# Performance work log

Measured on AMD Instinct MI355X. Metric: run time of the kernel, lower is better.

Reference implementation:

```python
import jax, jax.numpy as jnp
import numpy as np

OUT_FEATURES = 8192
IN_FEATURES = 8192
BATCH = 512


def setup_inputs() -> dict:
    key = jax.random.key(0)
    k_x, k_w, k_s = jax.random.split(key, 3)
    x = jax.random.normal(k_x, (BATCH, IN_FEATURES), dtype=jnp.float32)
    # packed int4 weights: each int holds two nibbles (values 0..255)
    packed_weight = jax.random.randint(k_w, (OUT_FEATURES, IN_FEATURES // 2), 0, 256, dtype=jnp.int32)
    # per-output-row scale (positive, as produced by abs-max quantization)
    scale = jax.random.uniform(k_s, (OUT_FEATURES, 1), dtype=jnp.float32) * 0.02 + 1e-4
    return {"x": x, "packed_weight": packed_weight, "scale": scale}


def reference(x, packed_weight, scale):
    # Unpack two 4-bit values per byte: high nibble first (matches torch loop:
    # col i <- packed >> 4 & 15, col i+1 <- packed & 15), then subtract zero-point 8.
    hi = (packed_weight >> 4) & 15
    lo = packed_weight & 15
    q = jnp.stack([hi, lo], axis=-1).reshape(OUT_FEATURES, IN_FEATURES) - 8  # [out, in] int
    w = q.astype(scale.dtype) * scale  # dequantized weight [out, in]
    # linear: y = x @ W^T
    return jnp.einsum('bi,oi->bo', x, w)
```

## Files before the change

### kernel.cpp

```cpp
#include <hip/hip_runtime.h>
#include <cstdint>
#include <cstddef>

#define IN_F 8192
#define OUT_F 8192
#define BATCH 512
#define KSPLIT 4
#define KSLICE (IN_F / KSPLIT)
#define BK 64
#define TILES (KSLICE / BK)
#define BM 256
#define BN 256

typedef __bf16 bf16x8 __attribute__((ext_vector_type(8)));
typedef float floatx4 __attribute__((ext_vector_type(4)));

__device__ __forceinline__ ushort f2bf(float f) {
  uint32_t u = __float_as_uint(f);
  u += 0x7FFFu + ((u >> 16) & 1u);
  return (ushort)(u >> 16);
}

__device__ __forceinline__ uint32_t dq(int p) {
  uint32_t u = (uint32_t)p;
  return (((u >> 4) & 0xFu) | ((u & 0xFu) << 16)) | 0x43004300u;
}

__device__ __forceinline__ void gl16(const void* g, uint32_t* l) {
  __builtin_amdgcn_global_load_lds(
      (const __attribute__((address_space(1))) uint32_t*)g,
      (__attribute__((address_space(3))) uint32_t*)l, 16, 0, 0);
}

__global__ __launch_bounds__(256) void cvt_rowsum(const float* __restrict__ x,
                                                  ushort* __restrict__ xb,
                                                  float* __restrict__ rowsum,
                                                  float* __restrict__ out) {
  const int b = blockIdx.x;
  const int t = threadIdx.x;
  const float4* xr = (const float4*)(x + (size_t)b * IN_F);
  ushort4* xo = (ushort4*)(xb + (size_t)b * IN_F);
  float4 z = {0.f, 0.f, 0.f, 0.f};
  float4* orow = (float4*)(out + (size_t)b * OUT_F);
  float s[4] = {0.f, 0.f, 0.f, 0.f};
#pragma unroll
  for (int i = 0; i < 8; ++i) {
    float4 v = xr[i * 256 + t];
    ushort4 o;
    o.x = f2bf(v.x); o.y = f2bf(v.y); o.z = f2bf(v.z); o.w = f2bf(v.w);
    xo[i * 256 + t] = o;
    orow[i * 256 + t] = z;
    s[i >> 1] += __uint_as_float((uint32_t)o.x << 16) + __uint_as_float((uint32_t)o.y << 16)
               + __uint_as_float((uint32_t)o.z << 16) + __uint_as_float((uint32_t)o.w << 16);
  }
  __shared__ float red[4][4];
  const int lane = t & 63, wid = t >> 6;
#pragma unroll
  for (int j = 0; j < 4; ++j) {
    float v = s[j];
#pragma unroll
    for (int off = 32; off >= 1; off >>= 1) v += __shfl_down(v, off, 64);
    if (lane == 0) red[wid][j] = v;
  }
  __syncthreads();
  if (t < 4) rowsum[t * BATCH + b] = red[0][t] + red[1][t] + red[2][t] + red[3][t];
}

__global__ __launch_bounds__(512, 2) void qgemm(const ushort* __restrict__ xb,
                                                const int* __restrict__ pw,
                                                const float* __restrict__ scale,
                                                const float* __restrict__ rowsum,
                                                float* __restrict__ out) {
  __shared__ uint32_t As[2 * BM * 32];
  __shared__ uint32_t Bs[2 * BN * 32];

  const int tid = threadIdx.x;
  const int lane = tid & 63;
  const int w = tid >> 6;
  const int wm = w >> 2, wn = w & 3;
  const int lr = lane & 15, lq = lane >> 4;

  const int n0 = blockIdx.x * BN;
  const int m0 = blockIdx.y * BM;
  const int ks = blockIdx.z;

  const char* aSrc = (const char*)xb
      + (size_t)(m0 + w * 32 + (lane >> 3)) * (IN_F * 2)
      + (size_t)ks * (KSLICE * 2)
      + (size_t)((((lane & 7) ^ ((lane >> 3) & 7)) * 16));
  uint32_t* aDst = As + (w * 32) * 32;

  const int rt = tid >> 1;
  const int c0 = (tid & 1) * 2;
  const int rk = rt & 7;
  const int* bSrc = pw + (size_t)(n0 + rt) * (IN_F / 2) + ks * (KSLICE / 2);

  const int key = lr & 7;
  const int aOff = (wm * 128 + lr) * 32 + ((lq ^ key) * 4);
  const int bOff = (wn * 64 + lr) * 32 + ((lq ^ key) * 4);

  floatx4 acc[8][4] = {};

  auto stB = [&](int nb, int q, int4 p) {
    int4 u;
    u.x = dq(p.x); u.y = dq(p.y); u.z = dq(p.z); u.w = dq(p.w);
    *(int4*)(Bs + nb * 8192 + rt * 32 + ((q ^ rk) * 4)) = u;
  };

#define RD_BV(kh)                                                            \
  _Pragma("unroll") for (int fn = 0; fn < 4; ++fn)                           \
      bv[fn] = *(const bf16x8*)(Bs + (((bOff + fn * 512) ^ ((kh)*16)) + buf * 8192));
#define RD_AV(mh, kh)                                                        \
  _Pragma("unroll") for (int fm = 0; fm < 4; ++fm)                           \
      av[fm] = *(const bf16x8*)(As + (((aOff + (mh)*2048 + fm * 512) ^ ((kh)*16)) + buf * 8192));
#define MFMA_BLK(mh)                                                         \
  __builtin_amdgcn_s_setprio(1);                                             \
  _Pragma("unroll") for (int fm = 0; fm < 4; ++fm)                           \
      _Pragma("unroll") for (int fn = 0; fn < 4; ++fn)                       \
          acc[(mh)*4 + fm][fn] = __builtin_amdgcn_mfma_f32_16x16x32_bf16(    \
              av[fm], bv[fn], acc[(mh)*4 + fm][fn], 0, 0, 0);                \
  __builtin_amdgcn_s_setprio(0);

  {
    int4 p0 = *(const int4*)(bSrc + c0 * 4);
    int4 p1 = *(const int4*)(bSrc + c0 * 4 + 4);
    int4 p2 = *(const int4*)(bSrc + (c0 + 4) * 4);
    int4 p3 = *(const int4*)(bSrc + (c0 + 4) * 4 + 4);
    stB(0, c0, p0); stB(0, c0 + 1, p1); stB(0, c0 + 4, p2); stB(0, c0 + 5, p3);
    gl16(aSrc, aDst);
    gl16(aSrc + 131072, aDst + 256);
    gl16(aSrc + 262144, aDst + 512);
    gl16(aSrc + 393216, aDst + 768);
    asm volatile("s_waitcnt lgkmcnt(0)" ::: "memory");
  }

  for (int t = 0; t < TILES - 1; ++t) {
    const int buf = t & 1, nb = buf ^ 1;
    const int* bs = bSrc + (t + 1) * 32;
    int4 pb0 = *(const int4*)(bs + c0 * 4);
    int4 pb1 = *(const int4*)(bs + c0 * 4 + 4);
    int4 pb2 = *(const int4*)(bs + (c0 + 4) * 4);
    int4 pb3 = *(const int4*)(bs + (c0 + 4) * 4 + 4);
    const char* as = aSrc + (size_t)(t + 1) * 128;
    gl16(as, aDst + nb * 8192);
    gl16(as + 131072, aDst + nb * 8192 + 256);
    gl16(as + 262144, aDst + nb * 8192 + 512);
    gl16(as + 393216, aDst + nb * 8192 + 768);
    asm volatile("s_waitcnt vmcnt(8)" ::: "memory");
    asm volatile("s_barrier" ::: "memory");

    bf16x8 av[4], bv[4];
    RD_BV(0);
    RD_AV(0, 0); MFMA_BLK(0);
    stB(nb, c0, pb0); stB(nb, c0 + 1, pb1);
    RD_AV(1, 0); MFMA_BLK(1);
    RD_BV(1);
    RD_AV(0, 1); MFMA_BLK(0);
    stB(nb, c0 + 4, pb2); stB(nb, c0 + 5, pb3);
    RD_AV(1, 1); MFMA_BLK(1);

    asm volatile("s_waitcnt lgkmcnt(0)" ::: "memory");
    asm volatile("s_barrier" ::: "memory");
  }

  {
    const int buf = (TILES - 1) & 1;
    asm volatile("s_waitcnt vmcnt(0)" ::: "memory");
    asm volatile("s_barrier" ::: "memory");
    bf16x8 av[4], bv[4];
    RD_BV(0);
    RD_AV(0, 0); MFMA_BLK(0);
    RD_AV(1, 0); MFMA_BLK(1);
    RD_BV(1);
    RD_AV(0, 1); MFMA_BLK(0);
    RD_AV(1, 1); MFMA_BLK(1);
  }

  const int omb = m0 + wm * 128 + lq * 4;
  const int on = n0 + wn * 64 + lr;
  float scv[4];
#pragma unroll
  for (int fn = 0; fn < 4; ++fn) scv[fn] = scale[on + fn * 16];
  float rsv[8][4];
#pragma unroll
  for (int fmg = 0; fmg < 8; ++fmg)
#pragma unroll
    for (int rr = 0; rr < 4; ++rr)
      rsv[fmg][rr] = rowsum[ks * BATCH + omb + fmg * 16 + rr];

#pragma unroll
  for (int fmg = 0; fmg < 8; ++fmg)
#pragma unroll
    for (int fn = 0; fn < 4; ++fn) {
      const float s = scv[fn];
      float* op = out + (size_t)(omb + fmg * 16) * OUT_F + (on + fn * 16);
#pragma unroll
      for (int rr = 0; rr < 4; ++rr)
        atomicAdd(op + (size_t)rr * OUT_F, s * (acc[fmg][fn][rr] - 136.f * rsv[fmg][rr]));
    }
#undef RD_BV
#undef RD_AV
#undef MFMA_BLK
}

extern "C" void kernel_launch(void* const* d_in, const int* in_sizes, int n_in,
                              void* d_out, int out_size, void* d_ws, size_t ws_size,
                              hipStream_t stream) {
  const float* x = (const float*)d_in[0];
  const int* pw = (const int*)d_in[1];
  const float* scale = (const float*)d_in[2];
  float* out = (float*)d_out;

  ushort* xb = (ushort*)d_ws;
  float* rowsum = (float*)((char*)d_ws + (size_t)BATCH * IN_F * sizeof(ushort));

  cvt_rowsum<<<BATCH, 256, 0, stream>>>(x, xb, rowsum, out);
  dim3 grid(OUT_F / BN, BATCH / BM, KSPLIT);
  qgemm<<<grid, 512, 0, stream>>>(xb, pw, scale, rowsum, out);
}
```

Measured before the change: 302.4 us.

## Replace split-K atomics with plain partial stores and separate reduction kernel

```diff
diff --git a/kernel.cpp b/kernel.cpp
--- a/kernel.cpp
+++ b/kernel.cpp
@@ -5,11 +5,11 @@
 #define IN_F 8192
 #define OUT_F 8192
 #define BATCH 512
-#define KSPLIT 4
+#define KSPLIT 2
 #define KSLICE (IN_F / KSPLIT)
 #define BK 64
 #define TILES (KSLICE / BK)
-#define BM 256
+#define BM 128
 #define BN 256
 
 typedef __bf16 bf16x8 __attribute__((ext_vector_type(8)));
@@ -35,42 +35,44 @@
 __global__ __launch_bounds__(256) void cvt_rowsum(const float* __restrict__ x,
                                                   ushort* __restrict__ xb,
                                                   float* __restrict__ rowsum,
-                                                  float* __restrict__ out) {
+                                                  float* __restrict__ zout) {
   const int b = blockIdx.x;
   const int t = threadIdx.x;
   const float4* xr = (const float4*)(x + (size_t)b * IN_F);
   ushort4* xo = (ushort4*)(xb + (size_t)b * IN_F);
-  float4 z = {0.f, 0.f, 0.f, 0.f};
-  float4* orow = (float4*)(out + (size_t)b * OUT_F);
-  float s[4] = {0.f, 0.f, 0.f, 0.f};
+  float s[2] = {0.f, 0.f};
 #pragma unroll
   for (int i = 0; i < 8; ++i) {
     float4 v = xr[i * 256 + t];
     ushort4 o;
     o.x = f2bf(v.x); o.y = f2bf(v.y); o.z = f2bf(v.z); o.w = f2bf(v.w);
     xo[i * 256 + t] = o;
-    orow[i * 256 + t] = z;
-    s[i >> 1] += __uint_as_float((uint32_t)o.x << 16) + __uint_as_float((uint32_t)o.y << 16)
+    if (zout) {
+      float4 z = {0.f, 0.f, 0.f, 0.f};
+      ((float4*)(zout + (size_t)b * OUT_F))[i * 256 + t] = z;
+    }
+    s[i >> 2] += __uint_as_float((uint32_t)o.x << 16) + __uint_as_float((uint32_t)o.y << 16)
                + __uint_as_float((uint32_t)o.z << 16) + __uint_as_float((uint32_t)o.w << 16);
   }
-  __shared__ float red[4][4];
+  __shared__ float red[4][2];
   const int lane = t & 63, wid = t >> 6;
 #pragma unroll
-  for (int j = 0; j < 4; ++j) {
+  for (int j = 0; j < 2; ++j) {
     float v = s[j];
 #pragma unroll
     for (int off = 32; off >= 1; off >>= 1) v += __shfl_down(v, off, 64);
     if (lane == 0) red[wid][j] = v;
   }
   __syncthreads();
-  if (t < 4) rowsum[t * BATCH + b] = red[0][t] + red[1][t] + red[2][t] + red[3][t];
+  if (t < 2) rowsum[t * BATCH + b] = red[0][t] + red[1][t] + red[2][t] + red[3][t];
 }
 
 __global__ __launch_bounds__(512, 2) void qgemm(const ushort* __restrict__ xb,
                                                 const int* __restrict__ pw,
                                                 const float* __restrict__ scale,
                                                 const float* __restrict__ rowsum,
-                                                float* __restrict__ out) {
+                                                float* __restrict__ out,
+                                                float* __restrict__ part) {
   __shared__ uint32_t As[2 * BM * 32];
   __shared__ uint32_t Bs[2 * BN * 32];
 
@@ -85,10 +87,10 @@
   const int ks = blockIdx.z;
 
   const char* aSrc = (const char*)xb
-      + (size_t)(m0 + w * 32 + (lane >> 3)) * (IN_F * 2)
+      + (size_t)(m0 + w * 16 + (lane >> 3)) * (IN_F * 2)
       + (size_t)ks * (KSLICE * 2)
       + (size_t)((((lane & 7) ^ ((lane >> 3) & 7)) * 16));
-  uint32_t* aDst = As + (w * 32) * 32;
+  uint32_t* aDst = As + (w * 16) * 32;
 
   const int rt = tid >> 1;
   const int c0 = (tid & 1) * 2;
@@ -96,10 +98,10 @@
   const int* bSrc = pw + (size_t)(n0 + rt) * (IN_F / 2) + ks * (KSLICE / 2);
 
   const int key = lr & 7;
-  const int aOff = (wm * 128 + lr) * 32 + ((lq ^ key) * 4);
+  const int aOff = (wm * 64 + lr) * 32 + ((lq ^ key) * 4);
   const int bOff = (wn * 64 + lr) * 32 + ((lq ^ key) * 4);
 
-  floatx4 acc[8][4] = {};
+  floatx4 acc[4][4] = {};
 
   auto stB = [&](int nb, int q, int4 p) {
     int4 u;
@@ -110,15 +112,15 @@
 #define RD_BV(kh)                                                            \
   _Pragma("unroll") for (int fn = 0; fn < 4; ++fn)                           \
       bv[fn] = *(const bf16x8*)(Bs + (((bOff + fn * 512) ^ ((kh)*16)) + buf * 8192));
-#define RD_AV(mh, kh)                                                        \
+#define RD_AV(kh)                                                            \
   _Pragma("unroll") for (int fm = 0; fm < 4; ++fm)                           \
-      av[fm] = *(const bf16x8*)(As + (((aOff + (mh)*2048 + fm * 512) ^ ((kh)*16)) + buf * 8192));
-#define MFMA_BLK(mh)                                                         \
+      av[fm] = *(const bf16x8*)(As + (((aOff + fm * 512) ^ ((kh)*16)) + buf * 4096));
+#define MFMA_BLK()                                                           \
   __builtin_amdgcn_s_setprio(1);                                             \
   _Pragma("unroll") for (int fm = 0; fm < 4; ++fm)                           \
       _Pragma("unroll") for (int fn = 0; fn < 4; ++fn)                       \
-          acc[(mh)*4 + fm][fn] = __builtin_amdgcn_mfma_f32_16x16x32_bf16(    \
-              av[fm], bv[fn], acc[(mh)*4 + fm][fn], 0, 0, 0);                \
+          acc[fm][fn] = __builtin_amdgcn_mfma_f32_16x16x32_bf16(             \
+              av[fm], bv[fn], acc[fm][fn], 0, 0, 0);                         \
   __builtin_amdgcn_s_setprio(0);
 
   {
@@ -129,8 +131,6 @@
     stB(0, c0, p0); stB(0, c0 + 1, p1); stB(0, c0 + 4, p2); stB(0, c0 + 5, p3);
     gl16(aSrc, aDst);
     gl16(aSrc + 131072, aDst + 256);
-    gl16(aSrc + 262144, aDst + 512);
-    gl16(aSrc + 393216, aDst + 768);
     asm volatile("s_waitcnt lgkmcnt(0)" ::: "memory");
   }
 
@@ -142,22 +142,18 @@
     int4 pb2 = *(const int4*)(bs + (c0 + 4) * 4);
     int4 pb3 = *(const int4*)(bs + (c0 + 4) * 4 + 4);
     const char* as = aSrc + (size_t)(t + 1) * 128;
-    gl16(as, aDst + nb * 8192);
-    gl16(as + 131072, aDst + nb * 8192 + 256);
-    gl16(as + 262144, aDst + nb * 8192 + 512);
-    gl16(as + 393216, aDst + nb * 8192 + 768);
-    asm volatile("s_waitcnt vmcnt(8)" ::: "memory");
+    gl16(as, aDst + nb * 4096);
+    gl16(as + 131072, aDst + nb * 4096 + 256);
+    asm volatile("s_waitcnt vmcnt(6)" ::: "memory");
     asm volatile("s_barrier" ::: "memory");
 
     bf16x8 av[4], bv[4];
-    RD_BV(0);
-    RD_AV(0, 0); MFMA_BLK(0);
+    RD_BV(0); RD_AV(0);
+    MFMA_BLK();
+    RD_BV(1); RD_AV(1);
+    MFMA_BLK();
     stB(nb, c0, pb0); stB(nb, c0 + 1, pb1);
-    RD_AV(1, 0); MFMA_BLK(1);
-    RD_BV(1);
-    RD_AV(0, 1); MFMA_BLK(0);
     stB(nb, c0 + 4, pb2); stB(nb, c0 + 5, pb3);
-    RD_AV(1, 1); MFMA_BLK(1);
 
     asm volatile("s_waitcnt lgkmcnt(0)" ::: "memory");
     asm volatile("s_barrier" ::: "memory");
@@ -168,39 +164,65 @@
     asm volatile("s_waitcnt vmcnt(0)" ::: "memory");
     asm volatile("s_barrier" ::: "memory");
     bf16x8 av[4], bv[4];
-    RD_BV(0);
-    RD_AV(0, 0); MFMA_BLK(0);
-    RD_AV(1, 0); MFMA_BLK(1);
-    RD_BV(1);
-    RD_AV(0, 1); MFMA_BLK(0);
-    RD_AV(1, 1); MFMA_BLK(1);
-  }
-
-  const int omb = m0 + wm * 128 + lq * 4;
+    RD_BV(0); RD_AV(0);
+    MFMA_BLK();
+    RD_BV(1); RD_AV(1);
+    MFMA_BLK();
+  }
+
+  const int omb = m0 + wm * 64 + lq * 4;
   const int on = n0 + wn * 64 + lr;
   float scv[4];
 #pragma unroll
   for (int fn = 0; fn < 4; ++fn) scv[fn] = scale[on + fn * 16];
-  float rsv[8][4];
-#pragma unroll
-  for (int fmg = 0; fmg < 8; ++fmg)
+  float rsv[4][4];
+#pragma unroll
+  for (int mi = 0; mi < 4; ++mi)
 #pragma unroll
     for (int rr = 0; rr < 4; ++rr)
-      rsv[fmg][rr] = rowsum[ks * BATCH + omb + fmg * 16 + rr];
-
-#pragma unroll
-  for (int fmg = 0; fmg < 8; ++fmg)
-#pragma unroll
-    for (int fn = 0; fn < 4; ++fn) {
-      const float s = scv[fn];
-      float* op = out + (size_t)(omb + fmg * 16) * OUT_F + (on + fn * 16);
-#pragma unroll
-      for (int rr = 0; rr < 4; ++rr)
-        atomicAdd(op + (size_t)rr * OUT_F, s * (acc[fmg][fn][rr] - 136.f * rsv[fmg][rr]));
-    }
+      rsv[mi][rr] = rowsum[ks * BATCH + omb + mi * 16 + rr];
+
+  if (part) {
+    float* dst = ks ? part : out;
+#pragma unroll
+    for (int mi = 0; mi < 4; ++mi)
+#pragma unroll
+      for (int fn = 0; fn < 4; ++fn) {
+        const float s = scv[fn];
+        float* op = dst + (size_t)(omb + mi * 16) * OUT_F + (on + fn * 16);
+#pragma unroll
+        for (int rr = 0; rr < 4; ++rr)
+          op[(size_t)rr * OUT_F] = s * (acc[mi][fn][rr] - 136.f * rsv[mi][rr]);
+      }
+  } else {
+#pragma unroll
+    for (int mi = 0; mi < 4; ++mi)
+#pragma unroll
+      for (int fn = 0; fn < 4; ++fn) {
+        const float s = scv[fn];
+        float* op = out + (size_t)(omb + mi * 16) * OUT_F + (on + fn * 16);
+#pragma unroll
+        for (int rr = 0; rr < 4; ++rr)
+          atomicAdd(op + (size_t)rr * OUT_F, s * (acc[mi][fn][rr] - 136.f * rsv[mi][rr]));
+      }
+  }
 #undef RD_BV
 #undef RD_AV
 #undef MFMA_BLK
+}
+
+__global__ __launch_bounds__(256) void reduce_add(float* __restrict__ out,
+                                                  const float* __restrict__ part) {
+  const size_t n = (size_t)BATCH * OUT_F / 4;
+  float4* o4 = (float4*)out;
+  const float4* p4 = (const float4*)part;
+  for (size_t i = (size_t)blockIdx.x * 256 + threadIdx.x; i < n;
+       i += (size_t)gridDim.x * 256) {
+    float4 a = o4[i];
+    float4 b = p4[i];
+    a.x += b.x; a.y += b.y; a.z += b.z; a.w += b.w;
+    o4[i] = a;
+  }
 }
 
 extern "C" void kernel_launch(void* const* d_in, const int* in_sizes, int n_in,
@@ -212,9 +234,14 @@
   float* out = (float*)d_out;
 
   ushort* xb = (ushort*)d_ws;
-  float* rowsum = (float*)((char*)d_ws + (size_t)BATCH * IN_F * sizeof(ushort));
-
-  cvt_rowsum<<<BATCH, 256, 0, stream>>>(x, xb, rowsum, out);
+  float* rowsum = (float*)((char*)d_ws + (size_t)8 * 1024 * 1024);
+  const size_t need = (size_t)8 * 1024 * 1024 + 65536 + (size_t)BATCH * OUT_F * 4;
+  float* part = (ws_size >= need)
+      ? (float*)((char*)d_ws + (size_t)8 * 1024 * 1024 + 65536)
+      : nullptr;
+
+  cvt_rowsum<<<BATCH, 256, 0, stream>>>(x, xb, rowsum, part ? nullptr : out);
   dim3 grid(OUT_F / BN, BATCH / BM, KSPLIT);
-  qgemm<<<grid, 512, 0, stream>>>(xb, pw, scale, rowsum, out);
-}
+  qgemm<<<grid, 512, 0, stream>>>(xb, pw, scale, rowsum, out, part);
+  if (part) reduce_add<<<2048, 256, 0, stream>>>(out, part);
+}
```

New measurement: 304.8 us. No clear change (+0.8%).
